# Kernel tuning notes

Measured on AMD Instinct MI355X. Metric: run time of the kernel, lower is better.

## Reference

```python
import jax, jax.numpy as jnp
import numpy as np

BETA = 0.9       # snn.Leaky(beta=0.9)
THRESH = 1.0     # snntorch default threshold, reset_mechanism='subtract'


def setup_inputs() -> dict:
    key = jax.random.key(0)
    ks = jax.random.split(key, 7)
    B = 16384
    return {
        "x":  jax.random.normal(ks[0], (B, 1700), dtype=jnp.float32),
        "W1": jax.random.normal(ks[1], (64, 1700), dtype=jnp.float32) * 0.02,
        "b1": jax.random.normal(ks[2], (64,), dtype=jnp.float32) * 0.02,
        "W2": jax.random.normal(ks[3], (32, 64), dtype=jnp.float32) * 0.1,
        "b2": jax.random.normal(ks[4], (32,), dtype=jnp.float32) * 0.1,
        "W3": jax.random.normal(ks[5], (2, 32), dtype=jnp.float32) * 0.1,
        "b3": jax.random.normal(ks[6], (2,), dtype=jnp.float32) * 0.1,
        "num_steps": 20,
    }


def _lif_step(mem, cur):
    # snntorch Leaky: reset (subtract) based on previous mem crossing threshold,
    # then leaky integration of the new input current.
    reset = (mem > THRESH).astype(mem.dtype)
    return BETA * mem + cur - reset * THRESH


def reference(x, W1, b1, W2, b2, W3, b3, num_steps):
    B = x.shape[0]
    # Dropout is identity in eval mode; x is constant across steps, so cur1 is
    # loop-invariant and computed once (same math as the original loop).
    cur1 = x @ W1.T + b1                         # [B, 64]

    def step(carry, _):
        mem1, mem2 = carry
        mem1 = _lif_step(mem1, cur1)             # [B, 64]
        cur2 = mem1 @ W2.T + b2                  # [B, 32]
        mem2 = _lif_step(mem2, cur2)             # [B, 32]
        return (mem1, mem2), None

    init = (jnp.zeros((B, 64), x.dtype), jnp.zeros((B, 32), x.dtype))
    (mem1, mem2), _ = jax.lax.scan(step, init, None, length=num_steps)
    return mem2 @ W3.T + b3                      # [B, 2]
```

## Files before the change

### kernel.cpp

```cpp
#include <hip/hip_runtime.h>
#include <hip/hip_bf16.h>

typedef float f32x4 __attribute__((ext_vector_type(4)));
typedef short bf16x8 __attribute__((ext_vector_type(8)));

#define MFMA16 __builtin_amdgcn_mfma_f32_16x16x32_bf16

static constexpr int KDIM = 1700;
static constexpr int NKT  = 54;
static constexpr float BETA = 0.9f;
static constexpr float THRESH = 1.0f;

__device__ __forceinline__ void split_bf(float f, short& hi, short& lo) {
    __hip_bfloat16 h = __float2bfloat16(f);
    float r = f - __bfloat162float(h);
    __hip_bfloat16 l = __float2bfloat16(r);
    hi = (short)__builtin_bit_cast(unsigned short, h);
    lo = (short)__builtin_bit_cast(unsigned short, l);
}

__device__ __forceinline__ void split8(f32x4 a, f32x4 b, bf16x8& hi, bf16x8& lo) {
    #pragma unroll
    for (int i = 0; i < 4; ++i) { short h, l; split_bf(a[i], h, l); hi[i] = h; lo[i] = l; }
    #pragma unroll
    for (int i = 0; i < 4; ++i) { short h, l; split_bf(b[i], h, l); hi[4 + i] = h; lo[4 + i] = l; }
}

__global__ void w1_relayout(const float* __restrict__ W1,
                            short* __restrict__ WTh, short* __restrict__ WTl) {
    const int g    = blockIdx.x * 256 + threadIdx.x;
    const int kt   = g >> 8;
    const int nt   = (g >> 6) & 3;
    const int lane = g & 63;
    const int n    = nt * 16 + (lane & 15);
    const int kb   = kt * 32 + (lane >> 4) * 8;
    bf16x8 vh, vl;
    #pragma unroll
    for (int i = 0; i < 8; ++i) {
        const int k = kb + i;
        const float v = (k < KDIM) ? W1[n * KDIM + k] : 0.f;
        short h, l; split_bf(v, h, l);
        vh[i] = h; vl[i] = l;
    }
    *(bf16x8*)(WTh + (size_t)g * 8) = vh;
    *(bf16x8*)(WTl + (size_t)g * 8) = vl;
}

__global__ __launch_bounds__(256, 2) void snn_fused(
    const float* __restrict__ x,
    const short* __restrict__ WTh, const short* __restrict__ WTl,
    const float* __restrict__ b1, const float* __restrict__ W2,
    const float* __restrict__ b2, const float* __restrict__ W3,
    const float* __restrict__ b3, const int* __restrict__ nsp,
    float* __restrict__ out)
{
    __shared__ float red[4][32][68];
    const int tid = threadIdx.x;
    const int wid = tid >> 6;
    const int lane = tid & 63;
    const int l15 = lane & 15;
    const int g4  = lane >> 4;
    const int kg  = g4 * 8;
    const int rowBase = blockIdx.x * 32;

    {
        const int t0  = wid * 13 + (wid < 2 ? wid : 2);
        const int t1  = t0 + 14 - (wid >> 1);
        const int t1e = (wid == 3) ? 53 : t1;

        const float* xr0 = x + (size_t)(rowBase + l15) * KDIM + kg;
        const float* xr1 = xr0 + (size_t)16 * KDIM;

        f32x4 acc[2][4] = {};
        f32x4 p00 = *(const f32x4*)(xr0 + t0 * 32);
        f32x4 p01 = *(const f32x4*)(xr0 + t0 * 32 + 4);
        f32x4 p10 = *(const f32x4*)(xr1 + t0 * 32);
        f32x4 p11 = *(const f32x4*)(xr1 + t0 * 32 + 4);

        for (int t = t0; t < t1e; ++t) {
            f32x4 a00 = p00, a01 = p01, a10 = p10, a11 = p11;
            if (t + 1 < t1e) {
                p00 = *(const f32x4*)(xr0 + (t + 1) * 32);
                p01 = *(const f32x4*)(xr0 + (t + 1) * 32 + 4);
                p10 = *(const f32x4*)(xr1 + (t + 1) * 32);
                p11 = *(const f32x4*)(xr1 + (t + 1) * 32 + 4);
            }
            const short* wb = WTh + (size_t)t * 2048 + lane * 8;
            const short* wl = WTl + (size_t)t * 2048 + lane * 8;
            bf16x8 bh[4], bl[4];
            #pragma unroll
            for (int nt = 0; nt < 4; ++nt) {
                bh[nt] = *(const bf16x8*)(wb + nt * 512);
                bl[nt] = *(const bf16x8*)(wl + nt * 512);
            }
            bf16x8 ah0, al0, ah1, al1;
            split8(a00, a01, ah0, al0);
            split8(a10, a11, ah1, al1);
            #pragma unroll
            for (int nt = 0; nt < 4; ++nt) {
                acc[0][nt] = MFMA16(ah0, bh[nt], acc[0][nt], 0, 0, 0);
                acc[0][nt] = MFMA16(al0, bh[nt], acc[0][nt], 0, 0, 0);
                acc[0][nt] = MFMA16(ah0, bl[nt], acc[0][nt], 0, 0, 0);
                acc[1][nt] = MFMA16(ah1, bh[nt], acc[1][nt], 0, 0, 0);
                acc[1][nt] = MFMA16(al1, bh[nt], acc[1][nt], 0, 0, 0);
                acc[1][nt] = MFMA16(ah1, bl[nt], acc[1][nt], 0, 0, 0);
            }
        }
        if (wid == 3) {
            f32x4 a00 = {0,0,0,0}, a01 = {0,0,0,0}, a10 = {0,0,0,0}, a11 = {0,0,0,0};
            if (g4 == 0) {
                a00 = *(const f32x4*)(xr0 + 53 * 32);
                a10 = *(const f32x4*)(xr1 + 53 * 32);
            }
            const short* wb = WTh + (size_t)53 * 2048 + lane * 8;
            const short* wl = WTl + (size_t)53 * 2048 + lane * 8;
            bf16x8 bh[4], bl[4];
            #pragma unroll
            for (int nt = 0; nt < 4; ++nt) {
                bh[nt] = *(const bf16x8*)(wb + nt * 512);
                bl[nt] = *(const bf16x8*)(wl + nt * 512);
            }
            bf16x8 ah0, al0, ah1, al1;
            split8(a00, a01, ah0, al0);
            split8(a10, a11, ah1, al1);
            #pragma unroll
            for (int nt = 0; nt < 4; ++nt) {
                acc[0][nt] = MFMA16(ah0, bh[nt], acc[0][nt], 0, 0, 0);
                acc[0][nt] = MFMA16(al0, bh[nt], acc[0][nt], 0, 0, 0);
                acc[0][nt] = MFMA16(ah0, bl[nt], acc[0][nt], 0, 0, 0);
                acc[1][nt] = MFMA16(ah1, bh[nt], acc[1][nt], 0, 0, 0);
                acc[1][nt] = MFMA16(al1, bh[nt], acc[1][nt], 0, 0, 0);
                acc[1][nt] = MFMA16(ah1, bl[nt], acc[1][nt], 0, 0, 0);
            }
        }

        #pragma unroll
        for (int mt = 0; mt < 2; ++mt)
            #pragma unroll
            for (int nt = 0; nt < 4; ++nt)
                #pragma unroll
                for (int j = 0; j < 4; ++j)
                    red[wid][mt * 16 + g4 * 4 + j][nt * 16 + l15] = acc[mt][nt][j];
    }
    __syncthreads();

    {
        const int rr  = tid >> 3;
        const int seg = tid & 7;
        f32x4 s0 = *(const f32x4*)(b1 + seg * 8);
        f32x4 s1 = *(const f32x4*)(b1 + seg * 8 + 4);
        #pragma unroll
        for (int p = 0; p < 4; ++p) {
            s0 += *(const f32x4*)&red[p][rr][seg * 8];
            s1 += *(const f32x4*)&red[p][rr][seg * 8 + 4];
        }
        *(f32x4*)&red[0][rr][seg * 8]     = s0;
        *(f32x4*)&red[0][rr][seg * 8 + 4] = s1;
    }
    __syncthreads();
    if (wid >= 2) return;

    const int lrow = wid * 16 + l15;

    float c1[2][8], c1m1[2][8];
    #pragma unroll
    for (int kt = 0; kt < 2; ++kt) {
        f32x4 u0 = *(const f32x4*)&red[0][lrow][kt * 32 + kg];
        f32x4 u1 = *(const f32x4*)&red[0][lrow][kt * 32 + kg + 4];
        #pragma unroll
        for (int i = 0; i < 4; ++i) {
            c1[kt][i] = u0[i];     c1[kt][4 + i] = u1[i];
            c1m1[kt][i] = u0[i] - THRESH; c1m1[kt][4 + i] = u1[i] - THRESH;
        }
    }

    bf16x8 W2hf[2][2], W2lf[2][2];
    #pragma unroll
    for (int rt = 0; rt < 2; ++rt)
        #pragma unroll
        for (int kt = 0; kt < 2; ++kt) {
            const float* wp = W2 + (rt * 16 + l15) * 64 + kt * 32 + kg;
            split8(*(const f32x4*)wp, *(const f32x4*)(wp + 4), W2hf[rt][kt], W2lf[rt][kt]);
        }

    float b2v[2][4], b2m1[2][4], w3a[2][4], w3b[2][4];
    #pragma unroll
    for (int nt = 0; nt < 2; ++nt)
        #pragma unroll
        for (int j = 0; j < 4; ++j) {
            const int o = nt * 16 + g4 * 4 + j;
            b2v[nt][j]  = b2[o];
            b2m1[nt][j] = b2[o] - THRESH;
            w3a[nt][j] = W3[o];
            w3b[nt][j] = W3[32 + o];
        }

    float m1[2][8] = {};
    float m2[2][4] = {};
    const int ns = nsp[0];
    for (int s = 0; s < ns; ++s) {
        bf16x8 mh[2], ml[2];
        #pragma unroll
        for (int kt = 0; kt < 2; ++kt)
            #pragma unroll
            for (int i = 0; i < 8; ++i) {
                float m = m1[kt][i];
                m = __builtin_fmaf(BETA, m, (m > THRESH) ? c1m1[kt][i] : c1[kt][i]);
                m1[kt][i] = m;
                short h, l; split_bf(m, h, l);
                mh[kt][i] = h; ml[kt][i] = l;
            }
        f32x4 a2[2][2] = {};
        #pragma unroll
        for (int rt = 0; rt < 2; ++rt)
            #pragma unroll
            for (int kt = 0; kt < 2; ++kt) {
                a2[rt][kt] = MFMA16(W2hf[rt][kt], mh[kt], a2[rt][kt], 0, 0, 0);
                a2[rt][kt] = MFMA16(W2lf[rt][kt], mh[kt], a2[rt][kt], 0, 0, 0);
                a2[rt][kt] = MFMA16(W2hf[rt][kt], ml[kt], a2[rt][kt], 0, 0, 0);
            }
        #pragma unroll
        for (int nt = 0; nt < 2; ++nt) {
            f32x4 c2 = a2[nt][0] + a2[nt][1];
            #pragma unroll
            for (int j = 0; j < 4; ++j) {
                float m = m2[nt][j];
                m2[nt][j] = __builtin_fmaf(
                    BETA, m, c2[j] + ((m > THRESH) ? b2m1[nt][j] : b2v[nt][j]));
            }
        }
    }

    float p0 = 0.f, p1 = 0.f;
    #pragma unroll
    for (int nt = 0; nt < 2; ++nt)
        #pragma unroll
        for (int j = 0; j < 4; ++j) {
            p0 = __builtin_fmaf(m2[nt][j], w3a[nt][j], p0);
            p1 = __builtin_fmaf(m2[nt][j], w3b[nt][j], p1);
        }
    p0 += __shfl_xor(p0, 16); p0 += __shfl_xor(p0, 32);
    p1 += __shfl_xor(p1, 16); p1 += __shfl_xor(p1, 32);
    if (lane < 16) {
        const size_t row = rowBase + lrow;
        out[row * 2 + 0] = p0 + b3[0];
        out[row * 2 + 1] = p1 + b3[1];
    }
}

extern "C" void kernel_launch(void* const* d_in, const int* in_sizes, int n_in,
                              void* d_out, int out_size, void* d_ws, size_t ws_size,
                              hipStream_t stream) {
    const float* x  = (const float*)d_in[0];
    const float* W1 = (const float*)d_in[1];
    const float* b1 = (const float*)d_in[2];
    const float* W2 = (const float*)d_in[3];
    const float* b2 = (const float*)d_in[4];
    const float* W3 = (const float*)d_in[5];
    const float* b3 = (const float*)d_in[6];
    const int*   ns = (const int*)d_in[7];
    float* o = (float*)d_out;

    const int B = in_sizes[0] / KDIM;
    short* WTh  = (short*)d_ws;
    short* WTl  = WTh + (size_t)NKT * 2048;

    w1_relayout<<<NKT, 256, 0, stream>>>(W1, WTh, WTl);
    snn_fused<<<B / 32, 256, 0, stream>>>(x, WTh, WTl, b1, W2, b2, W3, b3, ns, o);
}
```

Baseline: 44.07 us.

## Pad K tiles to 56 and fully unroll layer-1 GEMM with multi-stage prefetch

The weight relayout is padded to 56 K-tiles so each of the four waves handles exactly 14 tiles. This removes the uneven split and the special tail block. The layer-1 loop is fully unrolled with a three-deep register prefetch of x and double-buffered weight fragments, to hide global-load latency behind the MFMAs. Out-of-range x loads are clamped to a valid address and rely on zero-padded weights to cancel them. The cost is higher register pressure and the padding's correctness depending on the relayout kernel zero-filling tiles 53-55.

After: 46.89 us. 6.4% more time.

```diff
diff --git a/kernel.cpp b/kernel.cpp
--- a/kernel.cpp
+++ b/kernel.cpp
@@ -7,7 +7,7 @@
 #define MFMA16 __builtin_amdgcn_mfma_f32_16x16x32_bf16
 
 static constexpr int KDIM = 1700;
-static constexpr int NKT  = 54;
+static constexpr int NKT2 = 56;
 static constexpr float BETA = 0.9f;
 static constexpr float THRESH = 1.0f;
 
@@ -62,86 +62,82 @@
     const int g4  = lane >> 4;
     const int kg  = g4 * 8;
     const int rowBase = blockIdx.x * 32;
-
-    {
-        const int t0  = wid * 13 + (wid < 2 ? wid : 2);
-        const int t1  = t0 + 14 - (wid >> 1);
-        const int t1e = (wid == 3) ? 53 : t1;
-
-        const float* xr0 = x + (size_t)(rowBase + l15) * KDIM + kg;
-        const float* xr1 = xr0 + (size_t)16 * KDIM;
-
-        f32x4 acc[2][4] = {};
-        f32x4 p00 = *(const f32x4*)(xr0 + t0 * 32);
-        f32x4 p01 = *(const f32x4*)(xr0 + t0 * 32 + 4);
-        f32x4 p10 = *(const f32x4*)(xr1 + t0 * 32);
-        f32x4 p11 = *(const f32x4*)(xr1 + t0 * 32 + 4);
-
-        for (int t = t0; t < t1e; ++t) {
-            f32x4 a00 = p00, a01 = p01, a10 = p10, a11 = p11;
-            if (t + 1 < t1e) {
-                p00 = *(const f32x4*)(xr0 + (t + 1) * 32);
-                p01 = *(const f32x4*)(xr0 + (t + 1) * 32 + 4);
-                p10 = *(const f32x4*)(xr1 + (t + 1) * 32);
-                p11 = *(const f32x4*)(xr1 + (t + 1) * 32 + 4);
-            }
-            const short* wb = WTh + (size_t)t * 2048 + lane * 8;
-            const short* wl = WTl + (size_t)t * 2048 + lane * 8;
-            bf16x8 bh[4], bl[4];
-            #pragma unroll
-            for (int nt = 0; nt < 4; ++nt) {
-                bh[nt] = *(const bf16x8*)(wb + nt * 512);
-                bl[nt] = *(const bf16x8*)(wl + nt * 512);
-            }
-            bf16x8 ah0, al0, ah1, al1;
-            split8(a00, a01, ah0, al0);
-            split8(a10, a11, ah1, al1);
-            #pragma unroll
-            for (int nt = 0; nt < 4; ++nt) {
-                acc[0][nt] = MFMA16(ah0, bh[nt], acc[0][nt], 0, 0, 0);
-                acc[0][nt] = MFMA16(al0, bh[nt], acc[0][nt], 0, 0, 0);
-                acc[0][nt] = MFMA16(ah0, bl[nt], acc[0][nt], 0, 0, 0);
-                acc[1][nt] = MFMA16(ah1, bh[nt], acc[1][nt], 0, 0, 0);
-                acc[1][nt] = MFMA16(al1, bh[nt], acc[1][nt], 0, 0, 0);
-                acc[1][nt] = MFMA16(ah1, bl[nt], acc[1][nt], 0, 0, 0);
-            }
-        }
-        if (wid == 3) {
-            f32x4 a00 = {0,0,0,0}, a01 = {0,0,0,0}, a10 = {0,0,0,0}, a11 = {0,0,0,0};
-            if (g4 == 0) {
-                a00 = *(const f32x4*)(xr0 + 53 * 32);
-                a10 = *(const f32x4*)(xr1 + 53 * 32);
-            }
-            const short* wb = WTh + (size_t)53 * 2048 + lane * 8;
-            const short* wl = WTl + (size_t)53 * 2048 + lane * 8;
-            bf16x8 bh[4], bl[4];
-            #pragma unroll
-            for (int nt = 0; nt < 4; ++nt) {
-                bh[nt] = *(const bf16x8*)(wb + nt * 512);
-                bl[nt] = *(const bf16x8*)(wl + nt * 512);
-            }
-            bf16x8 ah0, al0, ah1, al1;
-            split8(a00, a01, ah0, al0);
-            split8(a10, a11, ah1, al1);
-            #pragma unroll
-            for (int nt = 0; nt < 4; ++nt) {
-                acc[0][nt] = MFMA16(ah0, bh[nt], acc[0][nt], 0, 0, 0);
-                acc[0][nt] = MFMA16(al0, bh[nt], acc[0][nt], 0, 0, 0);
-                acc[0][nt] = MFMA16(ah0, bl[nt], acc[0][nt], 0, 0, 0);
-                acc[1][nt] = MFMA16(ah1, bh[nt], acc[1][nt], 0, 0, 0);
-                acc[1][nt] = MFMA16(al1, bh[nt], acc[1][nt], 0, 0, 0);
-                acc[1][nt] = MFMA16(ah1, bl[nt], acc[1][nt], 0, 0, 0);
-            }
-        }
-
-        #pragma unroll
-        for (int mt = 0; mt < 2; ++mt)
-            #pragma unroll
-            for (int nt = 0; nt < 4; ++nt)
-                #pragma unroll
-                for (int j = 0; j < 4; ++j)
-                    red[wid][mt * 16 + g4 * 4 + j][nt * 16 + l15] = acc[mt][nt][j];
-    }
+    const int t0  = wid * 14;
+
+    const float* xr0 = x + (size_t)(rowBase + l15) * KDIM;
+    const float* xr1 = xr0 + (size_t)16 * KDIM;
+    const short* pWh = WTh + (size_t)t0 * 2048 + lane * 8;
+    const short* pWl = WTl + (size_t)t0 * 2048 + lane * 8;
+
+    struct XB { f32x4 a0, a1, b0, b1; };
+    auto xload = [&](int t, XB& xb) {
+        const int k1 = t * 32 + kg;
+        const int k2 = k1 + 4;
+        const int kc1 = (k1 <= 1696) ? k1 : 1664;
+        const int kc2 = (k2 <= 1696) ? k2 : 1664;
+        xb.a0 = *(const f32x4*)(xr0 + kc1);
+        xb.a1 = *(const f32x4*)(xr0 + kc2);
+        xb.b0 = *(const f32x4*)(xr1 + kc1);
+        xb.b1 = *(const f32x4*)(xr1 + kc2);
+    };
+    auto wload = [&](int i, bf16x8* Wf) {
+        #pragma unroll
+        for (int nt = 0; nt < 4; ++nt) {
+            Wf[nt]     = *(const bf16x8*)(pWh + (size_t)i * 2048 + nt * 512);
+            Wf[4 + nt] = *(const bf16x8*)(pWl + (size_t)i * 2048 + nt * 512);
+        }
+    };
+
+    f32x4 acc[2][4] = {};
+    XB x0, x1, x2;
+    bf16x8 WA[8], WB[8];
+
+    wload(0, WA);
+    xload(t0 + 0, x0);
+    xload(t0 + 1, x1);
+    xload(t0 + 2, x2);
+
+#define GSTEP(I, XC, WC, WN)                                               \
+    {                                                                      \
+        if constexpr ((I) + 1 < 14) wload((I) + 1, WN);                    \
+        bf16x8 ah0, al0, ah1, al1;                                         \
+        split8(XC.a0, XC.a1, ah0, al0);                                    \
+        split8(XC.b0, XC.b1, ah1, al1);                                    \
+        if constexpr ((I) + 3 < 14) xload(t0 + (I) + 3, XC);               \
+        _Pragma("unroll")                                                  \
+        for (int nt = 0; nt < 4; ++nt) {                                   \
+            acc[0][nt] = MFMA16(ah0, WC[nt],     acc[0][nt], 0, 0, 0);     \
+            acc[0][nt] = MFMA16(al0, WC[nt],     acc[0][nt], 0, 0, 0);     \
+            acc[0][nt] = MFMA16(ah0, WC[4 + nt], acc[0][nt], 0, 0, 0);     \
+            acc[1][nt] = MFMA16(ah1, WC[nt],     acc[1][nt], 0, 0, 0);     \
+            acc[1][nt] = MFMA16(al1, WC[nt],     acc[1][nt], 0, 0, 0);     \
+            acc[1][nt] = MFMA16(ah1, WC[4 + nt], acc[1][nt], 0, 0, 0);     \
+        }                                                                  \
+    }
+
+    GSTEP(0,  x0, WA, WB)
+    GSTEP(1,  x1, WB, WA)
+    GSTEP(2,  x2, WA, WB)
+    GSTEP(3,  x0, WB, WA)
+    GSTEP(4,  x1, WA, WB)
+    GSTEP(5,  x2, WB, WA)
+    GSTEP(6,  x0, WA, WB)
+    GSTEP(7,  x1, WB, WA)
+    GSTEP(8,  x2, WA, WB)
+    GSTEP(9,  x0, WB, WA)
+    GSTEP(10, x1, WA, WB)
+    GSTEP(11, x2, WB, WA)
+    GSTEP(12, x0, WA, WB)
+    GSTEP(13, x1, WB, WA)
+#undef GSTEP
+
+    #pragma unroll
+    for (int mt = 0; mt < 2; ++mt)
+        #pragma unroll
+        for (int nt = 0; nt < 4; ++nt)
+            #pragma unroll
+            for (int j = 0; j < 4; ++j)
+                red[wid][mt * 16 + g4 * 4 + j][nt * 16 + l15] = acc[mt][nt][j];
     __syncthreads();
 
     {
@@ -263,8 +259,8 @@
 
     const int B = in_sizes[0] / KDIM;
     short* WTh  = (short*)d_ws;
-    short* WTl  = WTh + (size_t)NKT * 2048;
-
-    w1_relayout<<<NKT, 256, 0, stream>>>(W1, WTh, WTl);
+    short* WTl  = WTh + (size_t)NKT2 * 2048;
+
+    w1_relayout<<<NKT2, 256, 0, stream>>>(W1, WTh, WTl);
     snn_fused<<<B / 32, 256, 0, stream>>>(x, WTh, WTl, b1, W2, b2, W3, b3, ns, o);
 }
```
